# Kernel optimization log

Hardware: AMD Instinct MI355X
Metric: run time of the kernel (lower is better)

The kernel has to match this reference:

```python
import jax, jax.numpy as jnp
import numpy as np

B, S, E, H, NF, NH, NIT = 64, 1024, 1024, 2048, 8, 4, 10
TEMP, XNOISE, LR = 1.0, 0.1, 0.1

PNAMES = ['ce_w1','ce_b1','ce_g','ce_be','ce_w2','ce_b2',
          'tp_w1','tp_b1','tp_g','tp_be','tp_w2','tp_b2',
          'en_w1','en_b1','en_g','en_be','en_w2','en_b2','en_w3','en_b3',
          'rn_w1','rn_b1','rn_g','rn_be','rn_w2','rn_b2']

def _ln(x, g, b):
    m = x.mean(-1, keepdims=True)
    v = ((x - m) ** 2).mean(-1, keepdims=True)
    return (x - m) * jax.lax.rsqrt(v + 1e-5) * g + b

def setup_inputs() -> dict:
    key = jax.random.key(0)
    ks = iter(jax.random.split(key, 40))
    w = lambda shape: jax.random.normal(next(ks), shape, jnp.float32) * 0.02
    z = lambda n: jnp.zeros((n,), jnp.float32)
    o = lambda n: jnp.ones((n,), jnp.float32)
    return {
        'current_embeddings': jax.random.normal(next(ks), (B, S, E), jnp.float32),
        'future_true': jax.random.normal(next(ks), (B, NF, E), jnp.float32),
        'ce_w1': w((E, H)), 'ce_b1': z(H), 'ce_g': o(H), 'ce_be': z(H), 'ce_w2': w((H, H)), 'ce_b2': z(H),
        'tp_w1': w((H, H)), 'tp_b1': z(H), 'tp_g': o(H), 'tp_be': z(H), 'tp_w2': w((H, E * NF)), 'tp_b2': z(E * NF),
        'en_w1': w((2 * E, H)), 'en_b1': z(H), 'en_g': o(H), 'en_be': z(H),
        'en_w2': w((H, H // 2)), 'en_b2': z(H // 2), 'en_w3': w((H // 2, 1)), 'en_b3': z(1),
        'rn_w1': w((3 * E, H)), 'rn_b1': z(H), 'rn_g': o(H), 'rn_be': z(H), 'rn_w2': w((H, E)), 'rn_b2': z(E),
    }

def _energy(emb, ce, ftrue, p):
    # emb: (..., NF, E); ce: (..., E); eval-mode (no dropout). Loop over t in
    # the original is a plain sum/NF -> vectorized over the NF axis here.
    ce_b = jnp.broadcast_to(ce[..., None, :], emb.shape)
    x = jnp.concatenate([emb, ce_b], axis=-1)            # (..., NF, 2E)
    x = jax.nn.relu(_ln(x @ p['en_w1'] + p['en_b1'], p['en_g'], p['en_be']))
    x = jax.nn.relu(x @ p['en_w2'] + p['en_b2'])
    coherence = (x @ p['en_w3'] + p['en_b3'])[..., 0].mean(-1)
    diffs = emb[..., 1:, :] - emb[..., :-1, :]
    smoothness = jnp.sqrt((diffs ** 2).sum(-1)).mean(-1)
    supervision = ((emb - ftrue) ** 2).mean((-1, -2))
    return coherence + 0.1 * smoothness + supervision

def _forward(cur, ft, p):
    ctx = cur.mean(1)                                    # (B, E)
    h = jax.nn.relu(_ln(ctx @ p['ce_w1'] + p['ce_b1'], p['ce_g'], p['ce_be']))
    ctx_h = h @ p['ce_w2'] + p['ce_b2']                  # (B, H)
    t = jax.nn.relu(_ln(ctx_h @ p['tp_w1'] + p['tp_b1'], p['tp_g'], p['tp_be']))
    traj = (t @ p['tp_w2'] + p['tp_b2']).reshape(B, 1, NF, E)
    # n_hypotheses identical deterministic trajectories + exploration noise
    noise = jax.random.normal(jax.random.key(42), (B, NH, NF, E), traj.dtype) * XNOISE
    hyp = traj + noise                                   # (B, NH, NF, E)
    ctx_e = ctx_h[:, :E]                                 # context[:, :embed_dim]

    emb = hyp.reshape(B * NH, NF, E)
    ce_flat = jnp.broadcast_to(ctx_e[:, None, :], (B, NH, E)).reshape(B * NH, E)
    ce_tiled = jnp.broadcast_to(ce_flat[:, None, :], (B * NH, NF, E))

    def refine(x, it):
        # all t-updates read the same snapshot of x -> fully vectorized over t
        prev = jnp.concatenate([x[:, :1], x[:, :-1]], axis=1)
        nxt = jnp.concatenate([x[:, 1:], x[:, -1:]], axis=1)
        neighbor = (prev + nxt) * 0.5
        inp = jnp.concatenate([x, ce_tiled, neighbor], axis=-1)   # (BH, NF, 3E)
        u = jax.nn.relu(_ln(inp @ p['rn_w1'] + p['rn_b1'], p['rn_g'], p['rn_be']))
        u = u @ p['rn_w2'] + p['rn_b2']
        x = x - LR * u
        ns = jax.random.normal(jax.random.fold_in(jax.random.key(7), it), x.shape, x.dtype) * (XNOISE * 0.1)
        x = jnp.where(it < NIT - 1, x + ns, x)  # noise on all but last iter
        return x, None

    emb, _ = jax.lax.scan(refine, emb, jnp.arange(NIT))
    refined = emb.reshape(B, NH, NF, E)

    ce_h = jnp.broadcast_to(ctx_e[:, None, :], (B, NH, E))
    ft_h = jnp.broadcast_to(ft[:, None], (B, NH, NF, E))
    energies = _energy(refined, ce_h, ft_h, p)           # (B, NH)
    probs = jax.nn.softmax(-energies / TEMP, axis=1)
    predictions = (refined * probs[..., None, None]).sum(1)  # (B, NF, E)
    return predictions

def reference(current_embeddings, future_true, ce_w1, ce_b1, ce_g, ce_be, ce_w2, ce_b2,
              tp_w1, tp_b1, tp_g, tp_be, tp_w2, tp_b2,
              en_w1, en_b1, en_g, en_be, en_w2, en_b2, en_w3, en_b3,
              rn_w1, rn_b1, rn_g, rn_be, rn_w2, rn_b2):
    p = dict(zip(PNAMES, (ce_w1, ce_b1, ce_g, ce_be, ce_w2, ce_b2,
                          tp_w1, tp_b1, tp_g, tp_be, tp_w2, tp_b2,
                          en_w1, en_b1, en_g, en_be, en_w2, en_b2, en_w3, en_b3,
                          rn_w1, rn_b1, rn_g, rn_be, rn_w2, rn_b2)))
    return _forward(current_embeddings, future_true, p)
```

## Files before the change

kernel.cpp:

```cpp
#include <hip/hip_runtime.h>
#include <hip/hip_bf16.h>
#include <stdint.h>

#define B_ 64
#define S_ 1024
#define E_ 1024
#define H_ 2048
#define NF_ 8
#define NH_ 4
#define NIT_ 10

typedef __attribute__((ext_vector_type(8))) short vshort8;
typedef __attribute__((ext_vector_type(8))) __bf16 vbf16x8;
typedef __attribute__((ext_vector_type(4))) float vfloat4;

typedef const __attribute__((address_space(1))) void* gas1_t;
typedef __attribute__((address_space(3))) void* las3_t;
__device__ __forceinline__ void gload16(const void* g, void* l) {
  __builtin_amdgcn_global_load_lds((gas1_t)g, (las3_t)l, 16, 0, 0);
}

__device__ __forceinline__ uint32_t rotl32(uint32_t v, int n) { return (v << n) | (v >> (32 - n)); }

__device__ __forceinline__ void threefry2x32(uint32_t k0, uint32_t k1, uint32_t x0, uint32_t x1,
                                             uint32_t& o0, uint32_t& o1) {
  uint32_t ks2 = k0 ^ k1 ^ 0x1BD11BDAu;
  x0 += k0; x1 += k1;
#define TF_R(r) { x0 += x1; x1 = rotl32(x1, (r)); x1 ^= x0; }
  TF_R(13) TF_R(15) TF_R(26) TF_R(6)
  x0 += k1;  x1 += ks2 + 1u;
  TF_R(17) TF_R(29) TF_R(16) TF_R(24)
  x0 += ks2; x1 += k0 + 2u;
  TF_R(13) TF_R(15) TF_R(26) TF_R(6)
  x0 += k0;  x1 += k1 + 3u;
  TF_R(17) TF_R(29) TF_R(16) TF_R(24)
  x0 += k1;  x1 += ks2 + 4u;
  TF_R(13) TF_R(15) TF_R(26) TF_R(6)
  x0 += ks2; x1 += k0 + 5u;
#undef TF_R
  o0 = x0; o1 = x1;
}

__device__ __forceinline__ uint32_t tf_bits_part(uint32_t k0, uint32_t k1, uint32_t i) {
  uint32_t o0, o1;
  threefry2x32(k0, k1, 0u, i, o0, o1);
  return o0 ^ o1;
}

__device__ __forceinline__ float erfinv_f(float x) {
  float w = -log1pf(-x * x);
  float p;
  if (w < 5.0f) {
    w -= 2.5f;
    p = 2.81022636e-08f;
    p = 3.43273939e-07f + p * w;
    p = -3.5233877e-06f + p * w;
    p = -4.39150654e-06f + p * w;
    p = 0.00021858087f + p * w;
    p = -0.00125372503f + p * w;
    p = -0.00417768164f + p * w;
    p = 0.246640727f + p * w;
    p = 1.50140941f + p * w;
  } else {
    w = sqrtf(w) - 3.0f;
    p = -0.000200214257f;
    p = 0.000100950558f + p * w;
    p = 0.00134934322f + p * w;
    p = -0.00367342844f + p * w;
    p = 0.00573950773f + p * w;
    p = -0.0076224613f + p * w;
    p = 0.00943887047f + p * w;
    p = 1.00167406f + p * w;
    p = 2.83297682f + p * w;
  }
  return p * x;
}

__device__ __forceinline__ float bits_to_normal(uint32_t bits) {
  uint32_t fb = (bits >> 9) | 0x3F800000u;
  float f = __uint_as_float(fb) - 1.0f;
  const float lo = -0.99999994f;
  float u = fmaxf(lo, f * 2.0f + lo);
  return 1.41421356f * erfinv_f(u);
}

__device__ __forceinline__ void load_bf8(const __hip_bfloat16* p, float v[8]) {
  vshort8 s = *(const vshort8*)p;
#pragma unroll
  for (int j = 0; j < 8; ++j) {
    uint32_t b = ((uint32_t)(uint16_t)s[j]) << 16;
    v[j] = __uint_as_float(b);
  }
}

__global__ __launch_bounds__(256) void colmean_partial(const float* __restrict__ cur,
                                                       float* __restrict__ part) {
  int blk = blockIdx.x;
  int b = blk >> 3, c = blk & 7;
  int t = threadIdx.x;
  const float* base = cur + ((size_t)b * S_ + (size_t)c * 128) * E_;
  float4 s = {0.f, 0.f, 0.f, 0.f};
  for (int si = 0; si < 128; ++si) {
    float4 v = *(const float4*)(base + (size_t)si * E_ + t * 4);
    s.x += v.x; s.y += v.y; s.z += v.z; s.w += v.w;
  }
  *(float4*)(part + ((size_t)c * B_ + b) * E_ + t * 4) = s;
}

__global__ __launch_bounds__(256) void colmean_final_bf(const float* __restrict__ part,
                                                        __hip_bfloat16* __restrict__ ctxb) {
  int i = blockIdx.x * 256 + threadIdx.x;
  float s = 0.f;
#pragma unroll
  for (int c = 0; c < 8; ++c) s += part[(size_t)c * (B_ * E_) + i];
  ctxb[i] = __float2bfloat16(s * (1.0f / S_));
}

struct TD {
  const float* src;
  __hip_bfloat16* dst;
  int K, N;
  float scale;
  int base;
};
struct TDArr { TD d[11]; };

__global__ __launch_bounds__(256) void transpose_batch(TDArr a) {
  __shared__ float tile[32][33];
  int b = blockIdx.x;
  int e = 0;
#pragma unroll
  for (int i = 1; i < 11; ++i)
    if (b >= a.d[i].base) e = i;
  TD t = a.d[e];
  int lt = b - t.base;
  int ntn = t.N >> 5;
  int n0 = (lt % ntn) * 32, k0 = (lt / ntn) * 32;
  int tx = threadIdx.x & 31, ty = threadIdx.x >> 5;
  for (int r = ty; r < 32; r += 8) tile[r][tx] = t.src[(size_t)(k0 + r) * t.N + n0 + tx];
  __syncthreads();
  for (int r = ty; r < 32; r += 8)
    t.dst[(size_t)(n0 + r) * t.K + k0 + tx] = __float2bfloat16(tile[tx][r] * t.scale);
}

__global__ __launch_bounds__(256) void mfma_skinny(const __hip_bfloat16* __restrict__ A,
                                                   const __hip_bfloat16* __restrict__ Bt,
                                                   float* __restrict__ part,
                                                   int N, int K, int lda, int Kc) {
  __shared__ short AS[64 * 32];
  __shared__ short BS[128 * 32];
  int t = threadIdx.x;
  int lane = t & 63, wv = t >> 6;
  int n0 = blockIdx.x * 128;
  int kbeg = blockIdx.y * Kc;
  int wn = wv * 32;
  int lrow = lane & 15, kb = (lane >> 4) * 8;
  vfloat4 acc[4][2];
#pragma unroll
  for (int i = 0; i < 4; ++i)
#pragma unroll
    for (int j = 0; j < 2; ++j) acc[i][j] = (vfloat4){0.f, 0.f, 0.f, 0.f};
  const short* Ag = (const short*)A;
  const short* Bg = (const short*)Bt;
  int arow = lane >> 2;
  int acol = (lane & 3) * 8;
  for (int k0 = kbeg; k0 < kbeg + Kc; k0 += 32) {
    gload16(Ag + (size_t)(wv * 16 + arow) * lda + k0 + acol, &AS[(wv * 16) * 32]);
#pragma unroll
    for (int c = 0; c < 2; ++c)
      gload16(Bg + (size_t)(n0 + c * 64 + wv * 16 + arow) * K + k0 + acol,
              &BS[(c * 64 + wv * 16) * 32]);
    __syncthreads();
    vbf16x8 af[4], bq[2];
#pragma unroll
    for (int i = 0; i < 4; ++i) af[i] = *(const vbf16x8*)&AS[(i * 16 + lrow) * 32 + kb];
#pragma unroll
    for (int j = 0; j < 2; ++j) bq[j] = *(const vbf16x8*)&BS[(wn + j * 16 + lrow) * 32 + kb];
#pragma unroll
    for (int i = 0; i < 4; ++i)
#pragma unroll
      for (int j = 0; j < 2; ++j)
        acc[i][j] = __builtin_amdgcn_mfma_f32_16x16x32_bf16(af[i], bq[j], acc[i][j], 0, 0, 0);
    __syncthreads();
  }
  size_t zbase = (size_t)blockIdx.y * 64;
  int crow0 = (lane >> 4) * 4;
  int ccol0 = n0 + wn + lrow;
#pragma unroll
  for (int i = 0; i < 4; ++i) {
#pragma unroll
    for (int j = 0; j < 2; ++j) {
      int col = ccol0 + j * 16;
#pragma unroll
      for (int r = 0; r < 4; ++r) {
        int rowi = i * 16 + crow0 + r;
        part[(zbase + rowi) * N + col] = acc[i][j][r];
      }
    }
  }
}

__global__ __launch_bounds__(256) void reduce_bias_bf(const float* __restrict__ part,
                                                      const float* __restrict__ bias,
                                                      __hip_bfloat16* __restrict__ Cb,
                                                      int N, int SK) {
  int i = blockIdx.x * 256 + threadIdx.x;
  int col = i & (N - 1);
  float s = bias[col];
  for (int z = 0; z < SK; ++z) s += part[(size_t)z * 64 * N + i];
  Cb[i] = __float2bfloat16(s);
}

__global__ __launch_bounds__(256) void reduce_cterm(const float* __restrict__ part,
                                                    const float* __restrict__ rn_b1,
                                                    const float* __restrict__ en_b1,
                                                    float* __restrict__ out, int SK) {
  int i = blockIdx.x * 256 + threadIdx.x;
  int col = i & 4095;
  float s = (col < 2048) ? rn_b1[col] : en_b1[col - 2048];
  for (int z = 0; z < SK; ++z) s += part[(size_t)z * 64 * 4096 + i];
  out[i] = s;
}

__global__ __launch_bounds__(256) void ln2048red(const float* __restrict__ part,
                                                 const float* __restrict__ bias,
                                                 const float* __restrict__ g,
                                                 const float* __restrict__ be,
                                                 __hip_bfloat16* __restrict__ out, int SK) {
  __shared__ float red[256];
  int row = blockIdx.x, t = threadIdx.x;
  int j0 = t * 8;
  float v[8];
  *(float4*)&v[0] = *(const float4*)(bias + j0);
  *(float4*)&v[4] = *(const float4*)(bias + j0 + 4);
  for (int z = 0; z < SK; ++z) {
    const float* p = part + (size_t)z * 64 * 2048 + (size_t)row * 2048 + j0;
    float4 a0 = *(const float4*)p, a1 = *(const float4*)(p + 4);
    v[0] += a0.x; v[1] += a0.y; v[2] += a0.z; v[3] += a0.w;
    v[4] += a1.x; v[5] += a1.y; v[6] += a1.z; v[7] += a1.w;
  }
  float s = 0.f;
#pragma unroll
  for (int j = 0; j < 8; ++j) s += v[j];
  red[t] = s; __syncthreads();
  for (int k = 128; k > 0; k >>= 1) { if (t < k) red[t] += red[t + k]; __syncthreads(); }
  float mean = red[0] * (1.0f / 2048.0f);
  __syncthreads();
  float s2 = 0.f;
#pragma unroll
  for (int j = 0; j < 8; ++j) { float d = v[j] - mean; s2 += d * d; }
  red[t] = s2; __syncthreads();
  for (int k = 128; k > 0; k >>= 1) { if (t < k) red[t] += red[t + k]; __syncthreads(); }
  float rstd = rsqrtf(red[0] * (1.0f / 2048.0f) + 1e-5f);
  __hip_bfloat16 o[8];
#pragma unroll
  for (int j = 0; j < 8; ++j) {
    float y = (v[j] - mean) * rstd * g[j0 + j] + be[j0 + j];
    o[j] = __float2bfloat16(fmaxf(y, 0.f));
  }
  *(vshort8*)&out[(size_t)row * 2048 + j0] = *(vshort8*)o;
}

template <int NEIGH>
__global__ __launch_bounds__(256) void ln_comb(const __hip_bfloat16* __restrict__ G,
                                               const float* __restrict__ cterm, int cstride,
                                               const float* __restrict__ g,
                                               const float* __restrict__ be,
                                               __hip_bfloat16* __restrict__ out) {
  __shared__ float red[256];
  int row = blockIdx.x, t = threadIdx.x;
  int j0 = t * 8;
  const int GS = NEIGH ? 4096 : 2048;
  float v[8];
  load_bf8(G + (size_t)row * GS + j0, v);
  {
    const float* p = cterm + (size_t)(row >> 5) * cstride + j0;
    float4 a0 = *(const float4*)p, a1 = *(const float4*)(p + 4);
    v[0] += a0.x; v[1] += a0.y; v[2] += a0.z; v[3] += a0.w;
    v[4] += a1.x; v[5] += a1.y; v[6] += a1.z; v[7] += a1.w;
  }
  if (NEIGH) {
    int f = row & 7;
    int prow = (f == 0) ? row : row - 1;
    int nrow = (f == NF_ - 1) ? row : row + 1;
    float a[8], b[8];
    load_bf8(G + (size_t)prow * 4096 + 2048 + j0, a);
    load_bf8(G + (size_t)nrow * 4096 + 2048 + j0, b);
#pragma unroll
    for (int j = 0; j < 8; ++j) v[j] += a[j] + b[j];
  }
  float s = 0.f;
#pragma unroll
  for (int j = 0; j < 8; ++j) s += v[j];
  red[t] = s; __syncthreads();
  for (int k = 128; k > 0; k >>= 1) { if (t < k) red[t] += red[t + k]; __syncthreads(); }
  float mean = red[0] * (1.0f / 2048.0f);
  __syncthreads();
  float s2 = 0.f;
#pragma unroll
  for (int j = 0; j < 8; ++j) { float d = v[j] - mean; s2 += d * d; }
  red[t] = s2; __syncthreads();
  for (int k = 128; k > 0; k >>= 1) { if (t < k) red[t] += red[t + k]; __syncthreads(); }
  float rstd = rsqrtf(red[0] * (1.0f / 2048.0f) + 1e-5f);
  __hip_bfloat16 o[8];
#pragma unroll
  for (int j = 0; j < 8; ++j) {
    float y = (v[j] - mean) * rstd * g[j0 + j] + be[j0 + j];
    o[j] = __float2bfloat16(fmaxf(y, 0.f));
  }
  *(vshort8*)&out[(size_t)row * 2048 + j0] = *(vshort8*)o;
}

template <int MODE>
__global__ __launch_bounds__(256) void gemm_gl(const __hip_bfloat16* __restrict__ A,
                                               const __hip_bfloat16* __restrict__ Bt,
                                               const float* __restrict__ bias,
                                               float* __restrict__ Cout,
                                               __hip_bfloat16* __restrict__ Cbout,
                                               int M, int N, int K, int it) {
  __shared__ short Als[128 * 64];
  __shared__ short Bls[64 * 64];
  int t = threadIdx.x;
  int lane = t & 63, wv = t >> 6;
  int n0 = blockIdx.x * 64, m0 = blockIdx.y * 128;
  int wm = (wv >> 1) * 64, wn = (wv & 1) * 32;
  int lrow = lane & 15, kb = (lane >> 4) * 8;
  vfloat4 acc[4][2];
#pragma unroll
  for (int i = 0; i < 4; ++i)
#pragma unroll
    for (int j = 0; j < 2; ++j) acc[i][j] = (vfloat4){0.f, 0.f, 0.f, 0.f};
  const short* Ag = (const short*)A;
  const short* Bg = (const short*)Bt;
  int arow = lane >> 3;
  int acol = (lane & 7) * 8;
  for (int k0 = 0; k0 < K; k0 += 64) {
#pragma unroll
    for (int c = 0; c < 4; ++c)
      gload16(Ag + (size_t)(m0 + c * 32 + wv * 8 + arow) * K + k0 + acol,
              &Als[(c * 32 + wv * 8) * 64]);
#pragma unroll
    for (int c = 0; c < 2; ++c)
      gload16(Bg + (size_t)(n0 + c * 32 + wv * 8 + arow) * K + k0 + acol,
              &Bls[(c * 32 + wv * 8) * 64]);
    __syncthreads();
    vbf16x8 af[2][4], bq[2][2];
#pragma unroll
    for (int ks = 0; ks < 2; ++ks) {
#pragma unroll
      for (int i = 0; i < 4; ++i)
        af[ks][i] = *(const vbf16x8*)&Als[(wm + i * 16 + lrow) * 64 + ks * 32 + kb];
#pragma unroll
      for (int j = 0; j < 2; ++j)
        bq[ks][j] = *(const vbf16x8*)&Bls[(wn + j * 16 + lrow) * 64 + ks * 32 + kb];
    }
#pragma unroll
    for (int ks = 0; ks < 2; ++ks)
#pragma unroll
      for (int i = 0; i < 4; ++i)
#pragma unroll
        for (int j = 0; j < 2; ++j)
          acc[i][j] = __builtin_amdgcn_mfma_f32_16x16x32_bf16(af[ks][i], bq[ks][j], acc[i][j], 0, 0, 0);
    __syncthreads();
  }
  int crow0 = m0 + wm + (lane >> 4) * 4;
  int ccol0 = n0 + wn + lrow;
  if (MODE == 4) {
#pragma unroll
    for (int i = 0; i < 4; ++i) {
#pragma unroll
      for (int j = 0; j < 2; ++j) {
        int col = ccol0 + j * 16;
#pragma unroll
        for (int r = 0; r < 4; ++r)
          Cbout[(size_t)(crow0 + i * 16 + r) * N + col] = __float2bfloat16(acc[i][j][r]);
      }
    }
  } else {
#pragma unroll
    for (int i = 0; i < 4; ++i) {
#pragma unroll
      for (int j = 0; j < 2; ++j) {
        int col = ccol0 + j * 16;
        float bv = bias[col];
#pragma unroll
        for (int r = 0; r < 4; ++r) {
          float v = acc[i][j][r] + bv;
          if (MODE == 1) v = fmaxf(v, 0.f);
          Cout[(size_t)(crow0 + i * 16 + r) * N + col] = v;
        }
      }
    }
  }
}

template <int MODE>
__global__ __launch_bounds__(256) void gemm_gl32(const __hip_bfloat16* __restrict__ A,
                                                 const __hip_bfloat16* __restrict__ Bt,
                                                 const float* __restrict__ bias,
                                                 float* __restrict__ Cout,
                                                 __hip_bfloat16* __restrict__ Cbout,
                                                 int M, int N, int K, int it) {
  __shared__ short Als[128 * 64];
  __shared__ short Bls[32 * 64];
  int t = threadIdx.x;
  int lane = t & 63, wv = t >> 6;
  int n0 = blockIdx.x * 32, m0 = blockIdx.y * 128;
  int wm = wv * 32;
  int lrow = lane & 15, kb = (lane >> 4) * 8;
  vfloat4 acc[2][2];
#pragma unroll
  for (int i = 0; i < 2; ++i)
#pragma unroll
    for (int j = 0; j < 2; ++j) acc[i][j] = (vfloat4){0.f, 0.f, 0.f, 0.f};
  const short* Ag = (const short*)A;
  const short* Bg = (const short*)Bt;
  int arow = lane >> 3;
  int acol = (lane & 7) * 8;
  for (int k0 = 0; k0 < K; k0 += 64) {
#pragma unroll
    for (int c = 0; c < 4; ++c)
      gload16(Ag + (size_t)(m0 + c * 32 + wv * 8 + arow) * K + k0 + acol,
              &Als[(c * 32 + wv * 8) * 64]);
    gload16(Bg + (size_t)(n0 + wv * 8 + arow) * K + k0 + acol, &Bls[(wv * 8) * 64]);
    __syncthreads();
    vbf16x8 af[2][2], bq[2][2];
#pragma unroll
    for (int ks = 0; ks < 2; ++ks) {
#pragma unroll
      for (int i = 0; i < 2; ++i)
        af[ks][i] = *(const vbf16x8*)&Als[(wm + i * 16 + lrow) * 64 + ks * 32 + kb];
#pragma unroll
      for (int j = 0; j < 2; ++j)
        bq[ks][j] = *(const vbf16x8*)&Bls[(j * 16 + lrow) * 64 + ks * 32 + kb];
    }
#pragma unroll
    for (int ks = 0; ks < 2; ++ks)
#pragma unroll
      for (int i = 0; i < 2; ++i)
#pragma unroll
        for (int j = 0; j < 2; ++j)
          acc[i][j] = __builtin_amdgcn_mfma_f32_16x16x32_bf16(af[ks][i], bq[ks][j], acc[i][j], 0, 0, 0);
    __syncthreads();
  }
  int crow0 = m0 + wm + (lane >> 4) * 4;
  int ccol0 = n0 + lrow;
  if (MODE == 2) {
    uint32_t key0 = 0, key1 = 0;
    bool addn = (it < NIT_ - 1);
    if (addn) threefry2x32(0u, 7u, 0u, (uint32_t)it, key0, key1);
#pragma unroll
    for (int i = 0; i < 2; ++i) {
#pragma unroll
      for (int j = 0; j < 2; ++j) {
        int col = ccol0 + j * 16;
        float bv = bias[col];
#pragma unroll
        for (int r = 0; r < 4; ++r) {
          uint32_t idx = (uint32_t)(crow0 + i * 16 + r) * N + col;
          float xv = Cout[idx] - 0.1f * (acc[i][j][r] + bv);
          if (addn) xv += 0.01f * bits_to_normal(tf_bits_part(key0, key1, idx));
          Cout[idx] = xv;
          Cbout[idx] = __float2bfloat16(xv);
        }
      }
    }
  } else {
#pragma unroll
    for (int i = 0; i < 2; ++i) {
#pragma unroll
      for (int j = 0; j < 2; ++j) {
        int col = ccol0 + j * 16;
        float bv = bias[col];
#pragma unroll
        for (int r = 0; r < 4; ++r) {
          float v = acc[i][j][r] + bv;
          if (MODE == 1) v = fmaxf(v, 0.f);
          Cout[(size_t)(crow0 + i * 16 + r) * N + col] = v;
        }
      }
    }
  }
}

__global__ __launch_bounds__(256) void reduce_traj_noise(const float* __restrict__ part,
                                                         const float* __restrict__ bias,
                                                         float* __restrict__ x,
                                                         __hip_bfloat16* __restrict__ xb,
                                                         int SK) {
  int i = blockIdx.x * 256 + threadIdx.x;
  int fe = i & 8191;
  float s = bias[fe];
  for (int z = 0; z < SK; ++z) s += part[(size_t)z * 524288 + i];
  int b = i >> 13;
#pragma unroll
  for (int h = 0; h < NH_; ++h) {
    uint32_t xi = (uint32_t)(b * 32768 + h * 8192 + fe);
    float xv = s + 0.1f * bits_to_normal(tf_bits_part(0u, 42u, xi));
    x[xi] = xv;
    xb[xi] = __float2bfloat16(xv);
  }
}

__global__ __launch_bounds__(256) void energy_final2(const float* __restrict__ u,
                                                     const float* __restrict__ w3,
                                                     const float* __restrict__ b3,
                                                     const float* __restrict__ x,
                                                     const float* __restrict__ ft,
                                                     float* __restrict__ energ) {
  __shared__ float red[256];
  int bh = blockIdx.x, t = threadIdx.x;
  int b = bh >> 2;
  const float* ur = u + (size_t)bh * (NF_ * 1024);
  const float* xb = x + (size_t)bh * (NF_ * E_);
  const float* fb = ft + (size_t)b * (NF_ * E_);
  float c = 0.f;
  for (int i = t; i < NF_ * 1024; i += 256) c += ur[i] * w3[i & 1023];
  red[t] = c; __syncthreads();
  for (int k = 128; k > 0; k >>= 1) { if (t < k) red[t] += red[t + k]; __syncthreads(); }
  float coh = red[0] * (1.0f / NF_) + b3[0];
  __syncthreads();
  float sup = 0.f;
  for (int i = t; i < NF_ * E_; i += 256) { float d = xb[i] - fb[i]; sup += d * d; }
  red[t] = sup; __syncthreads();
  for (int k = 128; k > 0; k >>= 1) { if (t < k) red[t] += red[t + k]; __syncthreads(); }
  float supervision = red[0] / (NF_ * E_);
  float smooth = 0.f;
  for (int d = 0; d < NF_ - 1; ++d) {
    __syncthreads();
    float sd = 0.f;
    for (int e = t; e < E_; e += 256) {
      float df = xb[(d + 1) * E_ + e] - xb[d * E_ + e];
      sd += df * df;
    }
    red[t] = sd; __syncthreads();
    for (int k = 128; k > 0; k >>= 1) { if (t < k) red[t] += red[t + k]; __syncthreads(); }
    smooth += sqrtf(red[0]);
  }
  smooth *= (1.0f / (NF_ - 1));
  if (t == 0) energ[bh] = coh + 0.1f * smooth + supervision;
}

__global__ __launch_bounds__(256) void predict2(const float* __restrict__ x,
                                                const float* __restrict__ energ,
                                                float* __restrict__ out) {
  __shared__ float pr[NH_];
  int i = blockIdx.x * 256 + threadIdx.x;
  int b = i >> 13, fe = i & 8191;
  if (threadIdx.x == 0) {
    float e[NH_], m = -1e30f;
#pragma unroll
    for (int h = 0; h < NH_; ++h) { e[h] = -energ[b * NH_ + h]; m = fmaxf(m, e[h]); }
    float s = 0.f, p[NH_];
#pragma unroll
    for (int h = 0; h < NH_; ++h) { p[h] = expf(e[h] - m); s += p[h]; }
#pragma unroll
    for (int h = 0; h < NH_; ++h) pr[h] = p[h] / s;
  }
  __syncthreads();
  float s = 0.f;
#pragma unroll
  for (int h = 0; h < NH_; ++h) s += x[(size_t)(b * NH_ + h) * 8192 + fe] * pr[h];
  out[i] = s;
}

extern "C" void kernel_launch(void* const* d_in, const int* in_sizes, int n_in,
                              void* d_out, int out_size, void* d_ws, size_t ws_size,
                              hipStream_t stream) {
  const float* cur   = (const float*)d_in[0];
  const float* ftrue = (const float*)d_in[1];
  const float* ce_w1 = (const float*)d_in[2];
  const float* ce_b1 = (const float*)d_in[3];
  const float* ce_g  = (const float*)d_in[4];
  const float* ce_be = (const float*)d_in[5];
  const float* ce_w2 = (const float*)d_in[6];
  const float* ce_b2 = (const float*)d_in[7];
  const float* tp_w1 = (const float*)d_in[8];
  const float* tp_b1 = (const float*)d_in[9];
  const float* tp_g  = (const float*)d_in[10];
  const float* tp_be = (const float*)d_in[11];
  const float* tp_w2 = (const float*)d_in[12];
  const float* tp_b2 = (const float*)d_in[13];
  const float* en_w1 = (const float*)d_in[14];
  const float* en_b1 = (const float*)d_in[15];
  const float* en_g  = (const float*)d_in[16];
  const float* en_be = (const float*)d_in[17];
  const float* en_w2 = (const float*)d_in[18];
  const float* en_b2 = (const float*)d_in[19];
  const float* en_w3 = (const float*)d_in[20];
  const float* en_b3 = (const float*)d_in[21];
  const float* rn_w1 = (const float*)d_in[22];
  const float* rn_b1 = (const float*)d_in[23];
  const float* rn_g  = (const float*)d_in[24];
  const float* rn_be = (const float*)d_in[25];
  const float* rn_w2 = (const float*)d_in[26];
  const float* rn_b2 = (const float*)d_in[27];
  (void)in_sizes; (void)n_in; (void)out_size; (void)ws_size;

  char* w = (char*)d_ws;
  size_t off = 0;
  auto alloc = [&](size_t bytes) -> void* {
    void* p = w + off;
    off += (bytes + 255) & ~(size_t)255;
    return p;
  };
  float* part   = (float*)alloc((size_t)8 * B_ * E_ * 4);
  float* x      = (float*)alloc((size_t)2097152 * 4);
  float* skpart = (float*)alloc((size_t)16 * 64 * 8192 * 4);
  __hip_bfloat16* Gb = (__hip_bfloat16*)alloc((size_t)2048 * 4096 * 2);
  float* u      = (float*)alloc((size_t)2048 * 1024 * 4);
  __hip_bfloat16* ub   = (__hip_bfloat16*)alloc((size_t)2048 * 2048 * 2);
  __hip_bfloat16* x_b  = (__hip_bfloat16*)alloc((size_t)2048 * 1024 * 2);
  float* energ  = (float*)alloc((size_t)256 * 4);
  float* ctermcat = (float*)alloc((size_t)B_ * 4096 * 4);
  __hip_bfloat16* Wcat_t  = (__hip_bfloat16*)alloc((size_t)4096 * 1024 * 2);
  __hip_bfloat16* Wbcat_t = (__hip_bfloat16*)alloc((size_t)4096 * 1024 * 2);
  __hip_bfloat16* rn_w2t = (__hip_bfloat16*)alloc((size_t)1024 * 2048 * 2);
  __hip_bfloat16* en1a_t = (__hip_bfloat16*)alloc((size_t)2048 * 1024 * 2);
  __hip_bfloat16* en_w2t = (__hip_bfloat16*)alloc((size_t)1024 * 2048 * 2);
  __hip_bfloat16* ctx_b  = (__hip_bfloat16*)alloc((size_t)B_ * E_ * 2);
  __hip_bfloat16* ctxh_b = (__hip_bfloat16*)alloc((size_t)B_ * H_ * 2);
  __hip_bfloat16* lnb    = (__hip_bfloat16*)alloc((size_t)B_ * H_ * 2);
  __hip_bfloat16* cw1t = (__hip_bfloat16*)alloc((size_t)2048 * 1024 * 2);
  __hip_bfloat16* cw2t = (__hip_bfloat16*)alloc((size_t)2048 * 2048 * 2);
  __hip_bfloat16* tw1t = (__hip_bfloat16*)alloc((size_t)2048 * 2048 * 2);
  __hip_bfloat16* tw2t = (__hip_bfloat16*)alloc((size_t)8192 * 2048 * 2);

  colmean_partial<<<512, 256, 0, stream>>>(cur, part);
  colmean_final_bf<<<256, 256, 0, stream>>>(part, ctx_b);

  TDArr ta;
  int base = 0;
  auto set = [&](int idx, const float* src, __hip_bfloat16* dst, int K, int N, float sc) {
    ta.d[idx] = TD{src, dst, K, N, sc, base};
    base += (N >> 5) * (K >> 5);
  };
  set(0, rn_w1, Wcat_t, 1024, 2048, 1.0f);
  set(1, rn_w1 + (size_t)2048 * 2048, Wcat_t + (size_t)2048 * 1024, 1024, 2048, 0.5f);
  set(2, rn_w1 + (size_t)1024 * 2048, Wbcat_t, 1024, 2048, 1.0f);
  set(3, en_w1 + (size_t)1024 * 2048, Wbcat_t + (size_t)2048 * 1024, 1024, 2048, 1.0f);
  set(4, rn_w2, rn_w2t, 2048, 1024, 1.0f);
  set(5, en_w1, en1a_t, 1024, 2048, 1.0f);
  set(6, en_w2, en_w2t, 2048, 1024, 1.0f);
  set(7, ce_w1, cw1t, 1024, 2048, 1.0f);
  set(8, ce_w2, cw2t, 2048, 2048, 1.0f);
  set(9, tp_w1, tw1t, 2048, 2048, 1.0f);
  set(10, tp_w2, tw2t, 2048, 8192, 1.0f);
  transpose_batch<<<base, 256, 0, stream>>>(ta);

  mfma_skinny<<<dim3(16, 16), 256, 0, stream>>>(ctx_b, cw1t, skpart, 2048, 1024, 1024, 64);
  ln2048red<<<B_, 256, 0, stream>>>(skpart, ce_b1, ce_g, ce_be, lnb, 16);
  mfma_skinny<<<dim3(16, 16), 256, 0, stream>>>(lnb, cw2t, skpart, 2048, 2048, 2048, 128);
  reduce_bias_bf<<<512, 256, 0, stream>>>(skpart, ce_b2, ctxh_b, 2048, 16);
  mfma_skinny<<<dim3(16, 16), 256, 0, stream>>>(ctxh_b, tw1t, skpart, 2048, 2048, 2048, 128);
  ln2048red<<<B_, 256, 0, stream>>>(skpart, tp_b1, tp_g, tp_be, lnb, 16);
  mfma_skinny<<<dim3(64, 8), 256, 0, stream>>>(lnb, tw2t, skpart, 8192, 2048, 2048, 256);
  reduce_traj_noise<<<2048, 256, 0, stream>>>(skpart, tp_b2, x, x_b, 8);

  mfma_skinny<<<dim3(32, 8), 256, 0, stream>>>(ctxh_b, Wbcat_t, skpart, 4096, 1024, 2048, 128);
  reduce_cterm<<<1024, 256, 0, stream>>>(skpart, rn_b1, en_b1, ctermcat, 8);

  for (int it = 0; it < NIT_; ++it) {
    gemm_gl<4><<<dim3(64, 16), 256, 0, stream>>>(x_b, Wcat_t, nullptr, nullptr, Gb,
                                                 2048, 4096, 1024, 0);
    ln_comb<1><<<2048, 256, 0, stream>>>(Gb, ctermcat, 4096, rn_g, rn_be, ub);
    gemm_gl32<2><<<dim3(32, 16), 256, 0, stream>>>(ub, rn_w2t, rn_b2, x, x_b,
                                                   2048, 1024, 2048, it);
  }

  gemm_gl<4><<<dim3(32, 16), 256, 0, stream>>>(x_b, en1a_t, nullptr, nullptr, Gb,
                                               2048, 2048, 1024, 0);
  ln_comb<0><<<2048, 256, 0, stream>>>(Gb, ctermcat + 2048, 4096, en_g, en_be, ub);
  gemm_gl32<1><<<dim3(32, 16), 256, 0, stream>>>(ub, en_w2t, en_b2, u, nullptr,
                                                 2048, 1024, 2048, 0);
  energy_final2<<<256, 256, 0, stream>>>(u, en_w3, en_b3, x, ftrue, energ);
  predict2<<<2048, 256, 0, stream>>>(x, energ, (float*)d_out);
}
```

Baseline: 1.092 ms.

## Fold neighbor-average term into GEMM K dimension via concatenated x/neighbor input

The refine loop previously computed a GEMM with N=4096 (own weights plus neighbor weights) and summed the shifted neighbor outputs in the layernorm kernel. Now the GEMM2 epilogue writes both x and the averaged neighbor embedding (0.5*(prev+next)) into a combined bf16 buffer of width 2048. The first GEMM then runs with K=2048 and N=2048 against a concatenated weight matrix, and ln_comb no longer gathers neighbor rows. This drops the extra G traffic and the neighbor loads, and keeps the same FLOPs. In exchange it adds an LDS staging step and a sync in the GEMM epilogue. Neighbor rows must fall within the 128-row tile, which holds because groups of 8 are aligned.

New measurement: 1.164 ms. +6.6%, slower.

```diff
diff --git a/kernel.cpp b/kernel.cpp
--- a/kernel.cpp
+++ b/kernel.cpp
@@ -122,6 +122,8 @@
   int K, N;
   float scale;
   int base;
+  int dstld;
+  int dstoff;
 };
 struct TDArr { TD d[11]; };
 
@@ -140,7 +142,8 @@
   for (int r = ty; r < 32; r += 8) tile[r][tx] = t.src[(size_t)(k0 + r) * t.N + n0 + tx];
   __syncthreads();
   for (int r = ty; r < 32; r += 8)
-    t.dst[(size_t)(n0 + r) * t.K + k0 + tx] = __float2bfloat16(tile[tx][r] * t.scale);
+    t.dst[(size_t)(n0 + r) * t.dstld + t.dstoff + k0 + tx] =
+        __float2bfloat16(tile[tx][r] * t.scale);
 }
 
 __global__ __launch_bounds__(256) void mfma_skinny(const __hip_bfloat16* __restrict__ A,
@@ -261,7 +264,6 @@
   *(vshort8*)&out[(size_t)row * 2048 + j0] = *(vshort8*)o;
 }
 
-template <int NEIGH>
 __global__ __launch_bounds__(256) void ln_comb(const __hip_bfloat16* __restrict__ G,
                                                const float* __restrict__ cterm, int cstride,
                                                const float* __restrict__ g,
@@ -270,24 +272,13 @@
   __shared__ float red[256];
   int row = blockIdx.x, t = threadIdx.x;
   int j0 = t * 8;
-  const int GS = NEIGH ? 4096 : 2048;
   float v[8];
-  load_bf8(G + (size_t)row * GS + j0, v);
+  load_bf8(G + (size_t)row * 2048 + j0, v);
   {
     const float* p = cterm + (size_t)(row >> 5) * cstride + j0;
     float4 a0 = *(const float4*)p, a1 = *(const float4*)(p + 4);
     v[0] += a0.x; v[1] += a0.y; v[2] += a0.z; v[3] += a0.w;
     v[4] += a1.x; v[5] += a1.y; v[6] += a1.z; v[7] += a1.w;
-  }
-  if (NEIGH) {
-    int f = row & 7;
-    int prow = (f == 0) ? row : row - 1;
-    int nrow = (f == NF_ - 1) ? row : row + 1;
-    float a[8], b[8];
-    load_bf8(G + (size_t)prow * 4096 + 2048 + j0, a);
-    load_bf8(G + (size_t)nrow * 4096 + 2048 + j0, b);
-#pragma unroll
-    for (int j = 0; j < 8; ++j) v[j] += a[j] + b[j];
   }
   float s = 0.f;
 #pragma unroll
@@ -317,7 +308,7 @@
                                                const float* __restrict__ bias,
                                                float* __restrict__ Cout,
                                                __hip_bfloat16* __restrict__ Cbout,
-                                               int M, int N, int K, int it) {
+                                               int M, int N, int K, int lda) {
   __shared__ short Als[128 * 64];
   __shared__ short Bls[64 * 64];
   int t = threadIdx.x;
@@ -337,7 +328,7 @@
   for (int k0 = 0; k0 < K; k0 += 64) {
 #pragma unroll
     for (int c = 0; c < 4; ++c)
-      gload16(Ag + (size_t)(m0 + c * 32 + wv * 8 + arow) * K + k0 + acol,
+      gload16(Ag + (size_t)(m0 + c * 32 + wv * 8 + arow) * lda + k0 + acol,
               &Als[(c * 32 + wv * 8) * 64]);
 #pragma unroll
     for (int c = 0; c < 2; ++c)
@@ -446,9 +437,11 @@
   int crow0 = m0 + wm + (lane >> 4) * 4;
   int ccol0 = n0 + lrow;
   if (MODE == 2) {
+    float* lx = (float*)Als;
     uint32_t key0 = 0, key1 = 0;
     bool addn = (it < NIT_ - 1);
     if (addn) threefry2x32(0u, 7u, 0u, (uint32_t)it, key0, key1);
+    float xv_[2][2][4];
 #pragma unroll
     for (int i = 0; i < 2; ++i) {
 #pragma unroll
@@ -461,7 +454,29 @@
           float xv = Cout[idx] - 0.1f * (acc[i][j][r] + bv);
           if (addn) xv += 0.01f * bits_to_normal(tf_bits_part(key0, key1, idx));
           Cout[idx] = xv;
-          Cbout[idx] = __float2bfloat16(xv);
+          xv_[i][j][r] = xv;
+          lx[(crow0 - m0 + i * 16 + r) * 32 + (col - n0)] = xv;
+        }
+      }
+    }
+    __syncthreads();
+#pragma unroll
+    for (int i = 0; i < 2; ++i) {
+#pragma unroll
+      for (int j = 0; j < 2; ++j) {
+        int col = ccol0 + j * 16;
+        int lc = col - n0;
+#pragma unroll
+        for (int r = 0; r < 4; ++r) {
+          int grow = crow0 + i * 16 + r;
+          int lr = grow - m0;
+          int f = grow & 7;
+          int lp = (f == 0) ? lr : lr - 1;
+          int ln_ = (f == NF_ - 1) ? lr : lr + 1;
+          float y = 0.5f * (lx[lp * 32 + lc] + lx[ln_ * 32 + lc]);
+          size_t rb = (size_t)grow * 2048;
+          Cbout[rb + col] = __float2bfloat16(xv_[i][j][r]);
+          Cbout[rb + 1024 + col] = __float2bfloat16(y);
         }
       }
     }
@@ -486,7 +501,7 @@
 __global__ __launch_bounds__(256) void reduce_traj_noise(const float* __restrict__ part,
                                                          const float* __restrict__ bias,
                                                          float* __restrict__ x,
-                                                         __hip_bfloat16* __restrict__ xb,
+                                                         __hip_bfloat16* __restrict__ xy,
                                                          int SK) {
   int i = blockIdx.x * 256 + threadIdx.x;
   int fe = i & 8191;
@@ -498,8 +513,26 @@
     uint32_t xi = (uint32_t)(b * 32768 + h * 8192 + fe);
     float xv = s + 0.1f * bits_to_normal(tf_bits_part(0u, 42u, xi));
     x[xi] = xv;
-    xb[xi] = __float2bfloat16(xv);
-  }
+    xy[(size_t)(xi >> 10) * 2048 + (xi & 1023)] = __float2bfloat16(xv);
+  }
+}
+
+__global__ __launch_bounds__(256) void y_init(const float* __restrict__ x,
+                                              __hip_bfloat16* __restrict__ xy) {
+  int i = (blockIdx.x * 256 + threadIdx.x) * 8;
+  int row = i >> 10, e0 = i & 1023;
+  int f = row & 7;
+  int pr = (f == 0) ? row : row - 1;
+  int nr = (f == NF_ - 1) ? row : row + 1;
+  float a[8], b[8];
+  *(float4*)&a[0] = *(const float4*)&x[(size_t)pr * 1024 + e0];
+  *(float4*)&a[4] = *(const float4*)&x[(size_t)pr * 1024 + e0 + 4];
+  *(float4*)&b[0] = *(const float4*)&x[(size_t)nr * 1024 + e0];
+  *(float4*)&b[4] = *(const float4*)&x[(size_t)nr * 1024 + e0 + 4];
+  __hip_bfloat16 o[8];
+#pragma unroll
+  for (int j = 0; j < 8; ++j) o[j] = __float2bfloat16(0.5f * (a[j] + b[j]));
+  *(vshort8*)&xy[(size_t)row * 2048 + 1024 + e0] = *(vshort8*)o;
 }
 
 __global__ __launch_bounds__(256) void energy_final2(const float* __restrict__ u,
@@ -607,13 +640,13 @@
   float* part   = (float*)alloc((size_t)8 * B_ * E_ * 4);
   float* x      = (float*)alloc((size_t)2097152 * 4);
   float* skpart = (float*)alloc((size_t)16 * 64 * 8192 * 4);
-  __hip_bfloat16* Gb = (__hip_bfloat16*)alloc((size_t)2048 * 4096 * 2);
+  __hip_bfloat16* Gb = (__hip_bfloat16*)alloc((size_t)2048 * 2048 * 2);
   float* u      = (float*)alloc((size_t)2048 * 1024 * 4);
   __hip_bfloat16* ub   = (__hip_bfloat16*)alloc((size_t)2048 * 2048 * 2);
-  __hip_bfloat16* x_b  = (__hip_bfloat16*)alloc((size_t)2048 * 1024 * 2);
+  __hip_bfloat16* xy_b = (__hip_bfloat16*)alloc((size_t)2048 * 2048 * 2);
   float* energ  = (float*)alloc((size_t)256 * 4);
   float* ctermcat = (float*)alloc((size_t)B_ * 4096 * 4);
-  __hip_bfloat16* Wcat_t  = (__hip_bfloat16*)alloc((size_t)4096 * 1024 * 2);
+  __hip_bfloat16* Wcat2_t = (__hip_bfloat16*)alloc((size_t)2048 * 2048 * 2);
   __hip_bfloat16* Wbcat_t = (__hip_bfloat16*)alloc((size_t)4096 * 1024 * 2);
   __hip_bfloat16* rn_w2t = (__hip_bfloat16*)alloc((size_t)1024 * 2048 * 2);
   __hip_bfloat16* en1a_t = (__hip_bfloat16*)alloc((size_t)2048 * 1024 * 2);
@@ -631,21 +664,22 @@
 
   TDArr ta;
   int base = 0;
-  auto set = [&](int idx, const float* src, __hip_bfloat16* dst, int K, int N, float sc) {
-    ta.d[idx] = TD{src, dst, K, N, sc, base};
+  auto set = [&](int idx, const float* src, __hip_bfloat16* dst, int K, int N, float sc,
+                 int dstld, int dstoff) {
+    ta.d[idx] = TD{src, dst, K, N, sc, base, dstld, dstoff};
     base += (N >> 5) * (K >> 5);
   };
-  set(0, rn_w1, Wcat_t, 1024, 2048, 1.0f);
-  set(1, rn_w1 + (size_t)2048 * 2048, Wcat_t + (size_t)2048 * 1024, 1024, 2048, 0.5f);
-  set(2, rn_w1 + (size_t)1024 * 2048, Wbcat_t, 1024, 2048, 1.0f);
-  set(3, en_w1 + (size_t)1024 * 2048, Wbcat_t + (size_t)2048 * 1024, 1024, 2048, 1.0f);
-  set(4, rn_w2, rn_w2t, 2048, 1024, 1.0f);
-  set(5, en_w1, en1a_t, 1024, 2048, 1.0f);
-  set(6, en_w2, en_w2t, 2048, 1024, 1.0f);
-  set(7, ce_w1, cw1t, 1024, 2048, 1.0f);
-  set(8, ce_w2, cw2t, 2048, 2048, 1.0f);
-  set(9, tp_w1, tw1t, 2048, 2048, 1.0f);
-  set(10, tp_w2, tw2t, 2048, 8192, 1.0f);
+  set(0, rn_w1, Wcat2_t, 1024, 2048, 1.0f, 2048, 0);
+  set(1, rn_w1 + (size_t)2048 * 2048, Wcat2_t, 1024, 2048, 1.0f, 2048, 1024);
+  set(2, rn_w1 + (size_t)1024 * 2048, Wbcat_t, 1024, 2048, 1.0f, 1024, 0);
+  set(3, en_w1 + (size_t)1024 * 2048, Wbcat_t + (size_t)2048 * 1024, 1024, 2048, 1.0f, 1024, 0);
+  set(4, rn_w2, rn_w2t, 2048, 1024, 1.0f, 2048, 0);
+  set(5, en_w1, en1a_t, 1024, 2048, 1.0f, 1024, 0);
+  set(6, en_w2, en_w2t, 2048, 1024, 1.0f, 2048, 0);
+  set(7, ce_w1, cw1t, 1024, 2048, 1.0f, 1024, 0);
+  set(8, ce_w2, cw2t, 2048, 2048, 1.0f, 2048, 0);
+  set(9, tp_w1, tw1t, 2048, 2048, 1.0f, 2048, 0);
+  set(10, tp_w2, tw2t, 2048, 8192, 1.0f, 2048, 0);
   transpose_batch<<<base, 256, 0, stream>>>(ta);
 
   mfma_skinny<<<dim3(16, 16), 256, 0, stream>>>(ctx_b, cw1t, skpart, 2048, 1024, 1024, 64);
@@ -655,22 +689,23 @@
   mfma_skinny<<<dim3(16, 16), 256, 0, stream>>>(ctxh_b, tw1t, skpart, 2048, 2048, 2048, 128);
   ln2048red<<<B_, 256, 0, stream>>>(skpart, tp_b1, tp_g, tp_be, lnb, 16);
   mfma_skinny<<<dim3(64, 8), 256, 0, stream>>>(lnb, tw2t, skpart, 8192, 2048, 2048, 256);
-  reduce_traj_noise<<<2048, 256, 0, stream>>>(skpart, tp_b2, x, x_b, 8);
+  reduce_traj_noise<<<2048, 256, 0, stream>>>(skpart, tp_b2, x, xy_b, 8);
+  y_init<<<1024, 256, 0, stream>>>(x, xy_b);
 
   mfma_skinny<<<dim3(32, 8), 256, 0, stream>>>(ctxh_b, Wbcat_t, skpart, 4096, 1024, 2048, 128);
   reduce_cterm<<<1024, 256, 0, stream>>>(skpart, rn_b1, en_b1, ctermcat, 8);
 
   for (int it = 0; it < NIT_; ++it) {
-    gemm_gl<4><<<dim3(64, 16), 256, 0, stream>>>(x_b, Wcat_t, nullptr, nullptr, Gb,
-                                                 2048, 4096, 1024, 0);
-    ln_comb<1><<<2048, 256, 0, stream>>>(Gb, ctermcat, 4096, rn_g, rn_be, ub);
-    gemm_gl32<2><<<dim3(32, 16), 256, 0, stream>>>(ub, rn_w2t, rn_b2, x, x_b,
+    gemm_gl<4><<<dim3(32, 16), 256, 0, stream>>>(xy_b, Wcat2_t, nullptr, nullptr, Gb,
+                                                 2048, 2048, 2048, 2048);
+    ln_comb<<<2048, 256, 0, stream>>>(Gb, ctermcat, 4096, rn_g, rn_be, ub);
+    gemm_gl32<2><<<dim3(32, 16), 256, 0, stream>>>(ub, rn_w2t, rn_b2, x, xy_b,
                                                    2048, 1024, 2048, it);
   }
 
-  gemm_gl<4><<<dim3(32, 16), 256, 0, stream>>>(x_b, en1a_t, nullptr, nullptr, Gb,
-                                               2048, 2048, 1024, 0);
-  ln_comb<0><<<2048, 256, 0, stream>>>(Gb, ctermcat + 2048, 4096, en_g, en_be, ub);
+  gemm_gl<4><<<dim3(32, 16), 256, 0, stream>>>(xy_b, en1a_t, nullptr, nullptr, Gb,
+                                               2048, 2048, 1024, 2048);
+  ln_comb<<<2048, 256, 0, stream>>>(Gb, ctermcat + 2048, 4096, en_g, en_be, ub);
   gemm_gl32<1><<<dim3(32, 16), 256, 0, stream>>>(ub, en_w2t, en_b2, u, nullptr,
                                                  2048, 1024, 2048, 0);
   energy_final2<<<256, 256, 0, stream>>>(u, en_w3, en_b3, x, ftrue, energ);
```
